# Performance work log

Hardware: AMD Instinct MI355X
Metric: run time of the kernel (lower is better)

The kernel has to match this reference:

```python
import jax, jax.numpy as jnp
import numpy as np

B, T, P, D = 32, 8, 196, 768
M = 10
NUM_CLASSES = 100
NUM_IDX = 98
P_MASK = 0.5


def setup_inputs() -> dict:
    key = jax.random.key(0)
    ks = jax.random.split(key, 16)
    s = 0.02
    inp = {
        'visual': jax.random.normal(ks[0], (B, T * P, D), jnp.float32),
        'audio': jax.random.normal(ks[1], (B, D), jnp.float32),
        'causal': jax.random.normal(ks[2], (B, M, D), jnp.float32),
        'random_mask': jax.random.uniform(ks[3], (B, T, P, D)) < P_MASK,
        'Wa': jax.random.normal(ks[4], (D, D), jnp.float32) * s,
        'ba': jnp.zeros((D,), jnp.float32),
        'Wv': jax.random.normal(ks[5], (D, D), jnp.float32) * s,
        'bv': jnp.zeros((D,), jnp.float32),
        'Waa': jax.random.normal(ks[6], (D, D), jnp.float32) * s,
        'baa': jnp.zeros((D,), jnp.float32),
        'Wav': jax.random.normal(ks[7], (D, D), jnp.float32) * s,
        'bav': jnp.zeros((D,), jnp.float32),
        'Wf': jax.random.normal(ks[8], (D, D), jnp.float32) * s,
        'bf': jnp.zeros((D,), jnp.float32),
        'Wf2': jax.random.normal(ks[9], (D, 1), jnp.float32) * s,
        'bf2': jnp.zeros((1,), jnp.float32),
        'Wc': jax.random.normal(ks[10], (D, NUM_CLASSES), jnp.float32) * s,
        'bc': jnp.zeros((NUM_CLASSES,), jnp.float32),
        'causal_param': jnp.zeros((1,), jnp.float32),
    }
    return inp


def reference(visual, audio, causal, random_mask, Wa, ba, Wv, bv, Waa, baa,
              Wav, bav, Wf, bf, Wf2, bf2, Wc, bc, causal_param):
    vis = visual.reshape(visual.shape[0], T, -1, D)  # [B,8,196,768]

    # causal_intervention_mean_feature4
    cp = jax.nn.sigmoid(causal_param)                 # soft_clamp2, [1]
    feats = causal @ Wf + bf                          # [B,M,D]
    feats2 = jnp.swapaxes(causal @ Wf2 + bf2, 1, 2)   # [B,1,M]
    fw = jax.nn.softmax(jnp.tanh(feats), axis=1)      # [B,M,D]
    ci = jnp.einsum('bom,bmd->bd', feats2, fw * causal)  # bmm + squeeze
    audio2 = cp * ci + audio                          # [B,D]

    # audio_visual_attention1
    pa = jnp.tanh(audio2 @ Waa + baa)                 # [B,D]
    pv = jnp.tanh(vis @ Wav + bav)                    # [B,T,P,D]
    sscore = pv * pa[:, None, None, :]                # einsum ijkd,id->ijkd
    sattn = jax.nn.softmax(sscore, axis=2)            # softmax over patches
    patch = jnp.sum(sattn, axis=-1)                   # [B,T,P]
    thresh = jnp.sort(patch, axis=-1)[:, :, NUM_IDX]  # per (b,t) threshold
    spa_mask = patch < thresh[:, :, None]             # [B,T,P]
    final_mask = ~(spa_mask[..., None] & random_mask) # [B,T,P,D]
    sfilt = jnp.where(final_mask, sattn, 0.0)

    sav = jnp.sum(sfilt * pv, axis=2)                 # [B,T,D]
    tattn = jax.nn.softmax(sav * pa[:, None, :], axis=1)

    vp = jnp.sum(sfilt * vis, axis=2)                 # [B,T,D]
    vp = jnp.sum(tattn * vp, axis=1)                  # [B,D]

    af = jax.nn.relu(audio2 @ Wa + ba)
    vf = jax.nn.relu(vp @ Wv + bv)
    logits = (af + vf) @ Wc + bc                      # [B,num_classes]
    return logits
```

## Files before the change

### kernel.cpp

```cpp
#include <hip/hip_runtime.h>
#include <hip/hip_bf16.h>
#include <hip/hip_fp16.h>
#include <math.h>

#define BB 32
#define TT 8
#define PP 196
#define DD 768
#define MM 10
#define NCLS 100
#define NIDX 98

typedef __attribute__((ext_vector_type(8))) short short8v;
typedef __attribute__((ext_vector_type(4))) float float4v;

__device__ __forceinline__ float fast_tanh(float x) {
    float e = __expf(2.0f * x);
    return 1.0f - 2.0f / (e + 1.0f);
}
__device__ __forceinline__ unsigned short f2bf(float x) {
    __hip_bfloat16 h = __float2bfloat16(x);
    return *(unsigned short*)&h;
}
__device__ __forceinline__ float bf2f(unsigned short h) {
    return __uint_as_float(((unsigned)h) << 16);
}
__device__ __forceinline__ unsigned short f2h(float x) {
    __half h = __float2half(x);
    return *(unsigned short*)&h;
}
__device__ __forceinline__ float h2f(unsigned short u) {
    __half h = *(__half*)&u;
    return __half2float(h);
}

__global__ __launch_bounds__(768) void k_prep_all(
    const float* __restrict__ vis, unsigned short* __restrict__ visb,
    const unsigned int* __restrict__ rm, int* __restrict__ mode,
    const float* __restrict__ Wav, unsigned short* __restrict__ Wht,
    const float* __restrict__ causal, const float* __restrict__ Wf,
    const float* __restrict__ Wf2,
    float* __restrict__ pf, float* __restrict__ pf2) {
    int t = threadIdx.x;
    int bid = blockIdx.x;
    if (bid < 1024) {
        const size_t NC = (size_t)BB * TT * PP * DD / 8;
        size_t gid = (size_t)bid * 768 + t;
        for (size_t i = gid; i < NC; i += 1024 * 768) {
            const float4* s = (const float4*)(vis + i * 8);
            float4 x = s[0], y = s[1];
            __hip_bfloat162 h;
            unsigned int u0, u1, u2, u3;
            h = __float22bfloat162_rn(make_float2(x.x, x.y)); u0 = *(unsigned int*)&h;
            h = __float22bfloat162_rn(make_float2(x.z, x.w)); u1 = *(unsigned int*)&h;
            h = __float22bfloat162_rn(make_float2(y.x, y.y)); u2 = *(unsigned int*)&h;
            h = __float22bfloat162_rn(make_float2(y.z, y.w)); u3 = *(unsigned int*)&h;
            uint4 o; o.x = u0; o.y = u1; o.z = u2; o.w = u3;
            ((uint4*)visb)[i] = o;
        }
        if (bid == 0) {
            __shared__ int f_ni, f_nf;
            if (t == 0) { f_ni = 0; f_nf = 0; }
            __syncthreads();
            int ni = 0, nf = 0;
            for (int i = t; i < 16384; i += 768) {
                unsigned int v = rm[i];
                ni |= (v > 1u) ? 1 : 0;
                nf |= (v != 0u && v != 0x3F800000u) ? 1 : 0;
            }
            if (ni) atomicOr(&f_ni, 1);
            if (nf) atomicOr(&f_nf, 1);
            __syncthreads();
            if (t == 0) *mode = f_ni ? (f_nf ? 2 : 1) : 0;
        }
    } else if (bid < 1600) {
        __shared__ float tile[32][33];
        int bb = bid - 1024;
        int bn = (bb % 24) * 32;
        int bk = (bb / 24) * 32;
        if (t < 256) {
            int tx = t & 31, ty = t >> 5;
            #pragma unroll
            for (int i = 0; i < 4; ++i)
                tile[ty + i * 8][tx] = Wav[(size_t)(bk + ty + i * 8) * DD + bn + tx];
        }
        __syncthreads();
        if (t < 256) {
            int tx = t & 31, ty = t >> 5;
            #pragma unroll
            for (int i = 0; i < 4; ++i) {
                int n = bn + ty + i * 8, k = bk + tx;
                Wht[(size_t)n * DD + k] = f2bf(tile[tx][ty + i * 8]);
            }
        }
    } else {
        __shared__ float cs[MM][256];
        __shared__ float red[MM][12];
        int bb = bid - 1600;
        int b = bb % 32, kc = bb / 32;
        int k0 = kc * 256;
        for (int i = t; i < MM * 256; i += 768)
            cs[i >> 8][i & 255] = causal[((size_t)b * MM + (i >> 8)) * DD + k0 + (i & 255)];
        __syncthreads();
        int wave = t >> 6, lane = t & 63;
        float w2v = (t < 256) ? Wf2[k0 + t] : 0.f;
        #pragma unroll
        for (int m = 0; m < MM; ++m) {
            float p = (t < 256) ? cs[m][t] * w2v : 0.f;
            #pragma unroll
            for (int o = 32; o > 0; o >>= 1) p += __shfl_down(p, o);
            if (lane == 0) red[m][wave] = p;
        }
        __syncthreads();
        if (t < MM) {
            float s = 0.f;
            #pragma unroll
            for (int wv = 0; wv < 4; ++wv) s += red[t][wv];
            pf2[(b * 3 + kc) * MM + t] = s;
        }
        float acc[MM];
        #pragma unroll
        for (int m = 0; m < MM; ++m) acc[m] = 0.f;
        #pragma unroll 4
        for (int k = 0; k < 256; ++k) {
            float wv = Wf[(size_t)(k0 + k) * DD + t];
            #pragma unroll
            for (int m = 0; m < MM; ++m) acc[m] = fmaf(cs[m][k], wv, acc[m]);
        }
        #pragma unroll
        for (int m = 0; m < MM; ++m)
            pf[(((size_t)b * 3 + kc) * MM + m) * DD + t] = acc[m];
    }
}

__global__ __launch_bounds__(768) void k_audio2a(
    const float* __restrict__ causal, const float* __restrict__ audio,
    const float* __restrict__ pf, const float* __restrict__ pf2,
    const float* __restrict__ bf, const float* __restrict__ bf2,
    const float* __restrict__ cparam, float* __restrict__ a2) {
    int b = blockIdx.x;
    int t = threadIdx.x;
    float cp = 1.0f / (1.0f + __expf(-cparam[0]));
    float tf[MM], f2[MM];
    float mx = -1e30f;
    #pragma unroll
    for (int m = 0; m < MM; ++m) {
        float acc = bf[t];
        float s2 = bf2[0];
        #pragma unroll
        for (int kc = 0; kc < 3; ++kc) {
            acc += pf[(((size_t)b * 3 + kc) * MM + m) * DD + t];
            s2 += pf2[(b * 3 + kc) * MM + m];
        }
        tf[m] = fast_tanh(acc);
        f2[m] = s2;
        mx = fmaxf(mx, tf[m]);
    }
    float s = 0.f;
    #pragma unroll
    for (int m = 0; m < MM; ++m) { tf[m] = __expf(tf[m] - mx); s += tf[m]; }
    float inv = 1.0f / s;
    float ci = 0.f;
    #pragma unroll
    for (int m = 0; m < MM; ++m)
        ci += f2[m] * (tf[m] * inv) * causal[((size_t)b * MM + m) * DD + t];
    a2[(size_t)b * DD + t] = cp * ci + audio[(size_t)b * DD + t];
}

__global__ __launch_bounds__(256) void k_audio2b(
    const float* __restrict__ a2,
    const float* __restrict__ Waa, const float* __restrict__ baa,
    const float* __restrict__ Wa, const float* __restrict__ ba,
    float* __restrict__ pa, float* __restrict__ af, float* __restrict__ colsum) {
    int gid0 = (blockIdx.y * 24 + blockIdx.x) * 256 + threadIdx.x;
    for (int i = gid0; i < BB * TT * DD; i += 48 * 256) colsum[i] = 0.f;
    __shared__ float a2s[16][DD + 4];
    int sel = blockIdx.y;
    const float* W = sel ? Wa : Waa;
    int t = threadIdx.x;
    int c = blockIdx.x * 32 + (t & 31);
    int slot = t >> 5;
    float bias = sel ? ba[c] : baa[c];
    #pragma unroll
    for (int g = 0; g < 2; ++g) {
        if (g) __syncthreads();
        for (int i = t; i < 16 * DD; i += 256)
            a2s[i / DD][i % DD] = a2[(size_t)(g * 16 + i / DD) * DD + i % DD];
        __syncthreads();
        float acc0 = 0.f, acc1 = 0.f;
        #pragma unroll 8
        for (int k = 0; k < DD; ++k) {
            float wv = W[(size_t)k * DD + c];
            acc0 = fmaf(a2s[slot][k], wv, acc0);
            acc1 = fmaf(a2s[slot + 8][k], wv, acc1);
        }
        int b0 = g * 16 + slot, b1 = b0 + 8;
        if (sel == 0) {
            pa[(size_t)b0 * DD + c] = fast_tanh(acc0 + bias);
            pa[(size_t)b1 * DD + c] = fast_tanh(acc1 + bias);
        } else {
            af[(size_t)b0 * DD + c] = fmaxf(acc0 + bias, 0.f);
            af[(size_t)b1 * DD + c] = fmaxf(acc1 + bias, 0.f);
        }
    }
}

__global__ __launch_bounds__(256, 4) void k_pv_mfma(
    const unsigned short* __restrict__ visb, const unsigned short* __restrict__ Wht,
    const float* __restrict__ bav, const float* __restrict__ pa,
    unsigned short* __restrict__ pvh, float* __restrict__ colsum)
{
    __shared__ unsigned short SH[4][4096];
    __shared__ float cred[256];
    int wg = blockIdx.x;
    int lin = (wg & 7) * 294 + (wg >> 3);
    int mt = lin / 6, nt = lin % 6;
    int i0 = mt * 128, n0 = nt * 128;
    int t = threadIdx.x, w = t >> 6, l = t & 63;
    int wm = (w >> 1) * 64, wn = (w & 1) * 64;

    float4v zero4 = {0.f, 0.f, 0.f, 0.f};
    float4v acc[4][4];
    #pragma unroll
    for (int a = 0; a < 4; ++a)
        #pragma unroll
        for (int b = 0; b < 4; ++b) acc[a][b] = zero4;

    int srow[2], scs[2];
    #pragma unroll
    for (int j = 0; j < 2; ++j) {
        int row = (w * 2 + j) * 16 + (l >> 2);
        srow[j] = row;
        scs[j] = (l & 3) ^ (row & 3);
    }

#define STAGE(bb, wnd_)                                                          \
    {                                                                            \
        int kw_ = (wnd_) * 32;                                                   \
        _Pragma("unroll")                                                        \
        for (int j = 0; j < 2; ++j) {                                            \
            size_t aoff_ = (size_t)(i0 + srow[j]) * DD + kw_ + scs[j] * 8;       \
            __builtin_amdgcn_global_load_lds(                                    \
                (const __attribute__((address_space(1))) unsigned int*)(visb + aoff_), \
                (__attribute__((address_space(3))) unsigned int*)&SH[bb][(w * 2 + j) * 512], \
                16, 0, 0);                                                       \
            size_t boff_ = (size_t)(n0 + srow[j]) * DD + kw_ + scs[j] * 8;       \
            __builtin_amdgcn_global_load_lds(                                    \
                (const __attribute__((address_space(1))) unsigned int*)(Wht + boff_), \
                (__attribute__((address_space(3))) unsigned int*)&SH[2 + bb][(w * 2 + j) * 512], \
                16, 0, 0);                                                       \
        }                                                                        \
    }

    STAGE(0, 0);
    for (int wnd = 0; wnd < 24; ++wnd) {
        int cur = wnd & 1;
        if (wnd < 23) {
            STAGE(cur ^ 1, wnd + 1);
            asm volatile("s_waitcnt vmcnt(4)" ::: "memory");
        } else {
            asm volatile("s_waitcnt vmcnt(0)" ::: "memory");
        }
        __builtin_amdgcn_s_barrier();
        __builtin_amdgcn_s_setprio(1);
        {
            short8v ahf[4], bhf[4];
            int cA = l >> 4;
            #pragma unroll
            for (int mr = 0; mr < 4; ++mr) {
                int row = wm + mr * 16 + (l & 15);
                ahf[mr] = *(const short8v*)&SH[cur][row * 32 + ((cA ^ (row & 3)) * 8)];
            }
            #pragma unroll
            for (int nc = 0; nc < 4; ++nc) {
                int row = wn + nc * 16 + (l & 15);
                bhf[nc] = *(const short8v*)&SH[2 + cur][row * 32 + ((cA ^ (row & 3)) * 8)];
            }
            #pragma unroll
            for (int mr = 0; mr < 4; ++mr)
                #pragma unroll
                for (int nc = 0; nc < 4; ++nc)
                    acc[mr][nc] = __builtin_amdgcn_mfma_f32_16x16x32_bf16(
                        ahf[mr], bhf[nc], acc[mr][nc], 0, 0, 0);
        }
        __builtin_amdgcn_s_setprio(0);
        asm volatile("s_waitcnt lgkmcnt(0)" ::: "memory");
        __builtin_amdgcn_sched_barrier(0);
        __builtin_amdgcn_s_barrier();
    }
#undef STAGE
    unsigned short* Cl = &SH[0][0];
    if (t < 256) cred[t] = 0.f;
    __syncthreads();
    int bt0 = i0 / PP;
    int btbound = (bt0 + 1) * PP;
    #pragma unroll
    for (int nc = 0; nc < 4; ++nc) {
        int cl = wn + nc * 16 + (l & 15);
        int col = n0 + cl;
        float bias = bav[col];
        #pragma unroll
        for (int mr = 0; mr < 4; ++mr) {
            int lr0 = wm + mr * 16 + ((l >> 4) << 2);
            int row0 = i0 + lr0;
            int bq = row0 / (TT * PP);
            float pav = pa[(size_t)bq * DD + col];
            float esum = 0.f;
            #pragma unroll
            for (int v = 0; v < 4; ++v) {
                unsigned short pb = f2h(fast_tanh(acc[mr][nc][v] + bias));
                int lr = lr0 + v;
                int boff = lr * 256 + ((cl * 2) ^ ((lr & 7) << 4));
                *(unsigned short*)((char*)Cl + boff) = pb;
                esum += __expf(h2f(pb) * pav);
            }
            int btg = (row0 >= btbound) ? 1 : 0;
            atomicAdd(&cred[btg * 128 + cl], esum);
        }
    }
    __syncthreads();
    #pragma unroll
    for (int rb = 0; rb < 2; ++rb) {
        int lr = (t >> 2) + rb * 64;
        size_t grow = (size_t)(i0 + lr) * DD + n0;
        #pragma unroll
        for (int q = 0; q < 4; ++q) {
            int ch = (t & 3) + q * 4;
            int boff = lr * 256 + ((ch * 16) ^ ((lr & 7) << 4));
            uint4 val = *(uint4*)((char*)Cl + boff);
            *(uint4*)(pvh + grow + ch * 8) = val;
        }
    }
    if (t < 256) {
        int btg = t >> 7, cl = t & 127;
        if (btg == 0 || btbound < i0 + 128)
            atomicAdd(&colsum[(size_t)(bt0 + btg) * DD + n0 + cl], cred[t]);
    }
}

__global__ __launch_bounds__(768) void k_patchsum(
    const unsigned short* __restrict__ pvh, const float* __restrict__ pa,
    const float* __restrict__ colsum, float* __restrict__ patch_q) {
    int bt = blockIdx.x, qd = blockIdx.y;
    int b = bt >> 3;
    size_t base = (size_t)bt * PP * DD;
    int c0 = qd * 192;
    __shared__ float2 pi[192];
    int t = threadIdx.x;
    if (t < 192) {
        int col = c0 + t;
        pi[t] = make_float2(pa[(size_t)b * DD + col],
                            1.0f / colsum[(size_t)bt * DD + col]);
    }
    __syncthreads();
    int wv = t >> 6, l = t & 63;
    for (int p = wv; p < PP; p += 12) {
        float sum = 0.f;
        if (l < 48) {
            const uint2* rv = (const uint2*)(pvh + base + (size_t)p * DD + c0);
            uint2 v = rv[l];
            int c = l * 4;
            float2 q0 = pi[c], q1 = pi[c + 1], q2 = pi[c + 2], q3 = pi[c + 3];
            sum = __expf(h2f((unsigned short)(v.x & 0xFFFFu)) * q0.x) * q0.y
                + __expf(h2f((unsigned short)(v.x >> 16)) * q1.x) * q1.y
                + __expf(h2f((unsigned short)(v.y & 0xFFFFu)) * q2.x) * q2.y
                + __expf(h2f((unsigned short)(v.y >> 16)) * q3.x) * q3.y;
        }
        #pragma unroll
        for (int o = 32; o > 0; o >>= 1) sum += __shfl_down(sum, o);
        if (l == 0) patch_q[((size_t)bt * PP + p) * 4 + qd] = sum;
    }
}

__global__ __launch_bounds__(768) void k_masked(
    const unsigned short* __restrict__ pvh, const unsigned short* __restrict__ visb,
    const void* __restrict__ rmask, const int* __restrict__ mode_p,
    const float* __restrict__ pa, const float* __restrict__ colsum,
    const float* __restrict__ patch_q,
    float* __restrict__ sav, float* __restrict__ vpt) {
    int bt = blockIdx.x;
    int qd = blockIdx.y;
    int b = bt >> 3;
    size_t base = (size_t)bt * PP * DD;
    __shared__ float patch[PP];
    __shared__ unsigned char spa[PP];
    __shared__ float red_s[4][192];
    __shared__ float red_v[4][192];
    int t = threadIdx.x;
    if (t < PP) {
        float4 v = *(const float4*)&patch_q[((size_t)bt * PP + t) * 4];
        patch[t] = ((v.x + v.y) + v.z) + v.w;
    }
    __syncthreads();
    if (t < PP) {
        float x = patch[t];
        int c = 0;
        for (int q = 0; q < PP; ++q) c += (patch[q] <= x) ? 1 : 0;
        spa[t] = (c <= NIDX) ? 1 : 0;
    }
    int pg = t / 192;
    int c = t - pg * 192;
    int col = qd * 192 + c;
    int p0 = pg * 49, p1 = p0 + 49;
    float pav = pa[(size_t)b * DD + col];
    float inv = 1.0f / colsum[(size_t)bt * DD + col];
    __syncthreads();
    const unsigned short* pvb = pvh + base + col;
    const unsigned short* vib = visb + base + col;
    float sava = 0.f, vpa = 0.f;
    int mode = *mode_p;
    if (mode == 0) {
        const int* mb = (const int*)rmask + base + col;
        #pragma unroll 7
        for (int p = p0; p < p1; ++p) {
            float pvv = h2f(pvb[(size_t)p * DD]);
            float sa = __expf(pvv * pav) * inv;
            bool km = !(spa[p] && (mb[(size_t)p * DD] != 0));
            if (km) { sava = fmaf(sa, pvv, sava); vpa = fmaf(sa, bf2f(vib[(size_t)p * DD]), vpa); }
        }
    } else if (mode == 1) {
        const float* mb = (const float*)rmask + base + col;
        #pragma unroll 7
        for (int p = p0; p < p1; ++p) {
            float pvv = h2f(pvb[(size_t)p * DD]);
            float sa = __expf(pvv * pav) * inv;
            bool km = !(spa[p] && (mb[(size_t)p * DD] != 0.f));
            if (km) { sava = fmaf(sa, pvv, sava); vpa = fmaf(sa, bf2f(vib[(size_t)p * DD]), vpa); }
        }
    } else {
        const unsigned char* mb = (const unsigned char*)rmask + base + col;
        #pragma unroll 7
        for (int p = p0; p < p1; ++p) {
            float pvv = h2f(pvb[(size_t)p * DD]);
            float sa = __expf(pvv * pav) * inv;
            bool km = !(spa[p] && (mb[(size_t)p * DD] != 0));
            if (km) { sava = fmaf(sa, pvv, sava); vpa = fmaf(sa, bf2f(vib[(size_t)p * DD]), vpa); }
        }
    }
    red_s[pg][c] = sava;
    red_v[pg][c] = vpa;
    __syncthreads();
    if (t < 192) {
        int col2 = qd * 192 + t;
        sav[(size_t)bt * DD + col2] = red_s[0][t] + red_s[1][t] + red_s[2][t] + red_s[3][t];
        vpt[(size_t)bt * DD + col2] = red_v[0][t] + red_v[1][t] + red_v[2][t] + red_v[3][t];
    }
}

__global__ __launch_bounds__(768) void k_tail_a(
    const float* __restrict__ sav, const float* __restrict__ vpt,
    const float* __restrict__ pa, float* __restrict__ vp) {
    int b = blockIdx.x;
    int t = threadIdx.x;
    float pav = pa[(size_t)b * DD + t];
    float x[TT];
    float mx = -1e30f;
    #pragma unroll
    for (int k = 0; k < TT; ++k) {
        x[k] = sav[((size_t)b * TT + k) * DD + t] * pav;
        mx = fmaxf(mx, x[k]);
    }
    float s = 0.f;
    #pragma unroll
    for (int k = 0; k < TT; ++k) { x[k] = __expf(x[k] - mx); s += x[k]; }
    float inv = 1.0f / s;
    float acc = 0.f;
    #pragma unroll
    for (int k = 0; k < TT; ++k)
        acc += x[k] * inv * vpt[((size_t)b * TT + k) * DD + t];
    vp[(size_t)b * DD + t] = acc;
}

__global__ __launch_bounds__(256) void k_tail_b(
    const float* __restrict__ vp, const float* __restrict__ af,
    const float* __restrict__ Wv, const float* __restrict__ bv,
    float* __restrict__ h) {
    __shared__ float vs[16][DD + 4];
    int t = threadIdx.x;
    int c = blockIdx.x * 32 + (t & 31);
    int slot = t >> 5;
    float bias = bv[c];
    #pragma unroll
    for (int g = 0; g < 2; ++g) {
        if (g) __syncthreads();
        for (int i = t; i < 16 * DD; i += 256)
            vs[i / DD][i % DD] = vp[(size_t)(g * 16 + i / DD) * DD + i % DD];
        __syncthreads();
        float acc0 = 0.f, acc1 = 0.f;
        #pragma unroll 8
        for (int k = 0; k < DD; ++k) {
            float wv = Wv[(size_t)k * DD + c];
            acc0 = fmaf(vs[slot][k], wv, acc0);
            acc1 = fmaf(vs[slot + 8][k], wv, acc1);
        }
        int b0 = g * 16 + slot, b1 = b0 + 8;
        h[(size_t)b0 * DD + c] = fmaxf(acc0 + bias, 0.f) + af[(size_t)b0 * DD + c];
        h[(size_t)b1 * DD + c] = fmaxf(acc1 + bias, 0.f) + af[(size_t)b1 * DD + c];
    }
}

__global__ __launch_bounds__(256) void k_tail_c(
    const float* __restrict__ h, const float* __restrict__ Wc,
    const float* __restrict__ bc, float* __restrict__ out) {
    int t = threadIdx.x;
    int c = blockIdx.x * 8 + (t & 7);
    int b = t >> 3;
    if (c >= NCLS) return;
    float acc = bc[c];
    #pragma unroll 8
    for (int k = 0; k < DD; ++k)
        acc = fmaf(h[(size_t)b * DD + k], Wc[(size_t)k * NCLS + c], acc);
    out[(size_t)b * NCLS + c] = acc;
}

extern "C" void kernel_launch(void* const* d_in, const int* in_sizes, int n_in,
                              void* d_out, int out_size, void* d_ws, size_t ws_size,
                              hipStream_t stream) {
    const float* visual = (const float*)d_in[0];
    const float* audio  = (const float*)d_in[1];
    const float* causal = (const float*)d_in[2];
    const void*  rmask  = d_in[3];
    const float* Wa   = (const float*)d_in[4];
    const float* ba   = (const float*)d_in[5];
    const float* Wv   = (const float*)d_in[6];
    const float* bv   = (const float*)d_in[7];
    const float* Waa  = (const float*)d_in[8];
    const float* baa  = (const float*)d_in[9];
    const float* Wav  = (const float*)d_in[10];
    const float* bav  = (const float*)d_in[11];
    const float* Wf   = (const float*)d_in[12];
    const float* bf   = (const float*)d_in[13];
    const float* Wf2  = (const float*)d_in[14];
    const float* bf2  = (const float*)d_in[15];
    const float* Wc   = (const float*)d_in[16];
    const float* bc   = (const float*)d_in[17];
    const float* cpar = (const float*)d_in[18];
    float* out = (float*)d_out;

    const size_t NE = (size_t)BB * TT * PP * DD;
    unsigned short* Wht = (unsigned short*)d_ws;
    float* pfreg = (float*)(Wht + (size_t)DD * DD);
    float* colsum = pfreg;
    float* savw  = colsum + (size_t)BB * TT * DD;
    float* vptw  = savw + (size_t)BB * TT * DD;
    float* vpw   = vptw + (size_t)BB * TT * DD;
    float* hw    = vpw + (size_t)BB * DD;
    float* pf    = pfreg;
    float* pf2   = pfreg + (size_t)BB * 3 * MM * DD;
    float* a2w   = pf2 + 1024;
    float* paw   = a2w + (size_t)BB * DD;
    float* afw   = paw + (size_t)BB * DD;
    int*   modew = (int*)(afw + (size_t)BB * DD);
    unsigned short* visb = (unsigned short*)(modew + 16);
    unsigned short* pvh  = visb + NE;
    float* patchq = (float*)(pvh + NE);

    k_prep_all<<<1696, 768, 0, stream>>>(visual, visb, (const unsigned int*)rmask,
                                         modew, Wav, Wht, causal, Wf, Wf2, pf, pf2);
    k_audio2a<<<BB, 768, 0, stream>>>(causal, audio, pf, pf2, bf, bf2, cpar, a2w);
    k_audio2b<<<dim3(24, 2), 256, 0, stream>>>(a2w, Waa, baa, Wa, ba, paw, afw, colsum);
    k_pv_mfma<<<2352, 256, 0, stream>>>(visb, Wht, bav, paw, pvh, colsum);
    k_patchsum<<<dim3(BB * TT, 4), 768, 0, stream>>>(pvh, paw, colsum, patchq);
    k_masked<<<dim3(BB * TT, 4), 768, 0, stream>>>(pvh, visb, rmask, modew, paw,
                                                   colsum, patchq, savw, vptw);
    k_tail_a<<<BB, 768, 0, stream>>>(savw, vptw, paw, vpw);
    k_tail_b<<<24, 256, 0, stream>>>(vpw, afw, Wv, bv, hw);
    k_tail_c<<<13, 256, 0, stream>>>(hw, Wc, bc, out);
}
```

Before: 509.7 us.

## Fuse three tail kernels into one per-batch kernel and change LDS swizzle

Merges the temporal softmax, the Wv projection with relu plus the audio term, and the classifier GEMV into a single kernel with one block per batch item, keeping vp and h in shared memory. This removes two launches and the global round trips for vp and h. In exchange each of the 32 blocks now streams the full Wv matrix, so Wv is read 32 times instead of being shared across batch rows, and the Wv work runs on only 32 workgroups. The LDS XOR swizzle in the MFMA GEMM now uses (row>>1)&3 instead of row&3, which is meant to reduce bank conflicts on the fragment reads.

```diff
diff --git a/kernel.cpp b/kernel.cpp
--- a/kernel.cpp
+++ b/kernel.cpp
@@ -231,7 +231,7 @@
     for (int j = 0; j < 2; ++j) {
         int row = (w * 2 + j) * 16 + (l >> 2);
         srow[j] = row;
-        scs[j] = (l & 3) ^ (row & 3);
+        scs[j] = (l & 3) ^ ((row >> 1) & 3);
     }
 
 #define STAGE(bb, wnd_)                                                          \
@@ -269,12 +269,12 @@
             #pragma unroll
             for (int mr = 0; mr < 4; ++mr) {
                 int row = wm + mr * 16 + (l & 15);
-                ahf[mr] = *(const short8v*)&SH[cur][row * 32 + ((cA ^ (row & 3)) * 8)];
+                ahf[mr] = *(const short8v*)&SH[cur][row * 32 + ((cA ^ ((row >> 1) & 3)) * 8)];
             }
             #pragma unroll
             for (int nc = 0; nc < 4; ++nc) {
                 int row = wn + nc * 16 + (l & 15);
-                bhf[nc] = *(const short8v*)&SH[2 + cur][row * 32 + ((cA ^ (row & 3)) * 8)];
+                bhf[nc] = *(const short8v*)&SH[2 + cur][row * 32 + ((cA ^ ((row >> 1) & 3)) * 8)];
             }
             #pragma unroll
             for (int mr = 0; mr < 4; ++mr)
@@ -447,11 +447,16 @@
     }
 }
 
-__global__ __launch_bounds__(768) void k_tail_a(
+__global__ __launch_bounds__(768) void k_tail(
     const float* __restrict__ sav, const float* __restrict__ vpt,
-    const float* __restrict__ pa, float* __restrict__ vp) {
+    const float* __restrict__ pa, const float* __restrict__ af,
+    const float* __restrict__ Wv, const float* __restrict__ bv,
+    const float* __restrict__ Wc, const float* __restrict__ bc,
+    float* __restrict__ out) {
     int b = blockIdx.x;
     int t = threadIdx.x;
+    __shared__ float vp[DD];
+    __shared__ float h[DD];
     float pav = pa[(size_t)b * DD + t];
     float x[TT];
     float mx = -1e30f;
@@ -468,49 +473,19 @@
     #pragma unroll
     for (int k = 0; k < TT; ++k)
         acc += x[k] * inv * vpt[((size_t)b * TT + k) * DD + t];
-    vp[(size_t)b * DD + t] = acc;
-}
-
-__global__ __launch_bounds__(256) void k_tail_b(
-    const float* __restrict__ vp, const float* __restrict__ af,
-    const float* __restrict__ Wv, const float* __restrict__ bv,
-    float* __restrict__ h) {
-    __shared__ float vs[16][DD + 4];
-    int t = threadIdx.x;
-    int c = blockIdx.x * 32 + (t & 31);
-    int slot = t >> 5;
-    float bias = bv[c];
-    #pragma unroll
-    for (int g = 0; g < 2; ++g) {
-        if (g) __syncthreads();
-        for (int i = t; i < 16 * DD; i += 256)
-            vs[i / DD][i % DD] = vp[(size_t)(g * 16 + i / DD) * DD + i % DD];
-        __syncthreads();
-        float acc0 = 0.f, acc1 = 0.f;
+    vp[t] = acc;
+    __syncthreads();
+    float accv = bv[t];
+    #pragma unroll 8
+    for (int k = 0; k < DD; ++k) accv = fmaf(vp[k], Wv[(size_t)k * DD + t], accv);
+    h[t] = fmaxf(accv, 0.f) + af[(size_t)b * DD + t];
+    __syncthreads();
+    if (t < NCLS) {
+        float accc = bc[t];
         #pragma unroll 8
-        for (int k = 0; k < DD; ++k) {
-            float wv = Wv[(size_t)k * DD + c];
-            acc0 = fmaf(vs[slot][k], wv, acc0);
-            acc1 = fmaf(vs[slot + 8][k], wv, acc1);
-        }
-        int b0 = g * 16 + slot, b1 = b0 + 8;
-        h[(size_t)b0 * DD + c] = fmaxf(acc0 + bias, 0.f) + af[(size_t)b0 * DD + c];
-        h[(size_t)b1 * DD + c] = fmaxf(acc1 + bias, 0.f) + af[(size_t)b1 * DD + c];
-    }
-}
-
-__global__ __launch_bounds__(256) void k_tail_c(
-    const float* __restrict__ h, const float* __restrict__ Wc,
-    const float* __restrict__ bc, float* __restrict__ out) {
-    int t = threadIdx.x;
-    int c = blockIdx.x * 8 + (t & 7);
-    int b = t >> 3;
-    if (c >= NCLS) return;
-    float acc = bc[c];
-    #pragma unroll 8
-    for (int k = 0; k < DD; ++k)
-        acc = fmaf(h[(size_t)b * DD + k], Wc[(size_t)k * NCLS + c], acc);
-    out[(size_t)b * NCLS + c] = acc;
+        for (int k = 0; k < DD; ++k) accc = fmaf(h[k], Wc[(size_t)k * NCLS + t], accc);
+        out[(size_t)b * NCLS + t] = accc;
+    }
 }
 
 extern "C" void kernel_launch(void* const* d_in, const int* in_sizes, int n_in,
@@ -543,8 +518,6 @@
     float* colsum = pfreg;
     float* savw  = colsum + (size_t)BB * TT * DD;
     float* vptw  = savw + (size_t)BB * TT * DD;
-    float* vpw   = vptw + (size_t)BB * TT * DD;
-    float* hw    = vpw + (size_t)BB * DD;
     float* pf    = pfreg;
     float* pf2   = pfreg + (size_t)BB * 3 * MM * DD;
     float* a2w   = pf2 + 1024;
@@ -563,7 +536,5 @@
     k_patchsum<<<dim3(BB * TT, 4), 768, 0, stream>>>(pvh, paw, colsum, patchq);
     k_masked<<<dim3(BB * TT, 4), 768, 0, stream>>>(pvh, visb, rmask, modew, paw,
                                                    colsum, patchq, savw, vptw);
-    k_tail_a<<<BB, 768, 0, stream>>>(savw, vptw, paw, vpw);
-    k_tail_b<<<24, 256, 0, stream>>>(vpw, afw, Wv, bv, hw);
-    k_tail_c<<<13, 256, 0, stream>>>(hw, Wc, bc, out);
-}
+    k_tail<<<BB, 768, 0, stream>>>(savw, vptw, paw, afw, Wv, bv, Wc, bc, out);
+}
```

New measurement: 479.5 us (median of 2 runs). 1.06x faster.
